# Optimization experiments

Hardware: AMD Instinct MI355X
Metric: run time of the kernel (lower is better)

Reference implementation:

```python
import jax, jax.numpy as jnp
import numpy as np

EPS = 1e-5
NHEAD = 8
NEG = -1e9  # matches -inf masked-fill semantics; rows never fully masked after fallback


def layer_norm(x, g, b):
    m = jnp.mean(x, axis=-1, keepdims=True)
    v = jnp.var(x, axis=-1, keepdims=True)
    return (x - m) * jax.lax.rsqrt(v + EPS) * g + b


def mha(q, k, v, Wqkv, bqkv, Wo, bo, bias=None):
    # torch nn.MultiheadAttention math (batch_first). Wqkv: [C, 3C] (jax layout).
    B, N, C = q.shape
    M = k.shape[1]
    d = C // NHEAD
    Wq, Wk, Wv = jnp.split(Wqkv, 3, axis=1)
    bq, bk, bv = jnp.split(bqkv, 3)
    qp = (q @ Wq + bq).reshape(B, N, NHEAD, d)
    kp = (k @ Wk + bk).reshape(B, M, NHEAD, d)
    vp = (v @ Wv + bv).reshape(B, M, NHEAD, d)
    s = jnp.einsum('bnhd,bmhd->bhnm', qp, kp) / np.sqrt(d).astype(q.dtype)
    if bias is not None:
        s = s + bias  # [B,1,N,M] broadcast over heads
    a = jax.nn.softmax(s, axis=-1)
    o = jnp.einsum('bhnm,bmhd->bnhd', a, vp).reshape(B, N, C)
    return o @ Wo + bo


def setup_inputs() -> dict:
    key = jax.random.key(0)
    B, Nq, HW, C, F = 8, 100, 4096, 512, 2048
    ks = jax.random.split(key, 16)
    s = 0.02
    inp = {
        'q': jax.random.normal(ks[0], (B, Nq, C), jnp.float32),
        'kv': jax.random.normal(ks[1], (B, HW, C), jnp.float32),
        'mask_bin': jax.random.randint(ks[2], (B, Nq, HW), 0, 2, jnp.int32),
        # MaskedXAttn: attn params + norm_q/norm_kv
        'xa_Wqkv': jax.random.normal(ks[3], (C, 3 * C), jnp.float32) * s,
        'xa_bqkv': jnp.zeros((3 * C,), jnp.float32),
        'xa_Wo': jax.random.normal(ks[4], (C, C), jnp.float32) * s,
        'xa_bo': jnp.zeros((C,), jnp.float32),
        'xa_gq': jnp.ones((C,), jnp.float32),
        'xa_bq_ln': jnp.zeros((C,), jnp.float32),
        'xa_gkv': jnp.ones((C,), jnp.float32),
        'xa_bkv_ln': jnp.zeros((C,), jnp.float32),
        # self-attention
        'sa_Wqkv': jax.random.normal(ks[5], (C, 3 * C), jnp.float32) * s,
        'sa_bqkv': jnp.zeros((3 * C,), jnp.float32),
        'sa_Wo': jax.random.normal(ks[6], (C, C), jnp.float32) * s,
        'sa_bo': jnp.zeros((C,), jnp.float32),
        # norms
        'n1_g': jnp.ones((C,), jnp.float32), 'n1_b': jnp.zeros((C,), jnp.float32),
        'n2_g': jnp.ones((C,), jnp.float32), 'n2_b': jnp.zeros((C,), jnp.float32),
        # FFN (MLP with num_layers=2: Linear(C,F), ReLU, Linear(F,C))
        'ff_W1': jax.random.normal(ks[7], (C, F), jnp.float32) * s,
        'ff_b1': jnp.zeros((F,), jnp.float32),
        'ff_W2': jax.random.normal(ks[8], (F, C), jnp.float32) * s,
        'ff_b2': jnp.zeros((C,), jnp.float32),
    }
    return inp


def reference(q, kv, mask_bin,
              xa_Wqkv, xa_bqkv, xa_Wo, xa_bo, xa_gq, xa_bq_ln, xa_gkv, xa_bkv_ln,
              sa_Wqkv, sa_bqkv, sa_Wo, sa_bo,
              n1_g, n1_b, n2_g, n2_b,
              ff_W1, ff_b1, ff_W2, ff_b2):
    # --- masked cross-attention (vectorized equivalent of per-query loop) ---
    qn = layer_norm(q, xa_gq, xa_bq_ln)
    kvn = layer_norm(kv, xa_gkv, xa_bkv_ln)
    allow = mask_bin.astype(bool)                      # [B,Nq,HW] True = attend
    row_any = jnp.any(allow, axis=-1, keepdims=True)   # queries with empty mask -> full attention
    eff = jnp.where(row_any, allow, True)
    bias = jnp.where(eff, 0.0, NEG).astype(q.dtype)[:, None, :, :]  # [B,1,Nq,HW]
    xa = mha(qn, kvn, kvn, xa_Wqkv, xa_bqkv, xa_Wo, xa_bo, bias=bias)
    q = q + xa
    # --- self-attention over queries ---
    qn1 = layer_norm(q, n1_g, n1_b)
    sa = mha(qn1, qn1, qn1, sa_Wqkv, sa_bqkv, sa_Wo, sa_bo)
    q = q + sa
    # --- FFN ---
    qn2 = layer_norm(q, n2_g, n2_b)
    h = jax.nn.relu(qn2 @ ff_W1 + ff_b1)
    q = q + (h @ ff_W2 + ff_b2)
    return q
```

## Files before the change

### kernel.cpp

```cpp
#include <hip/hip_runtime.h>

typedef unsigned short u16;
typedef unsigned int u32;
typedef __bf16 bf16x8 __attribute__((ext_vector_type(8)));
typedef short s16x4 __attribute__((ext_vector_type(4)));
typedef float f32x4 __attribute__((ext_vector_type(4)));

#define NEG_INF -3.0e38f
#define QSCALE 0.18033688011f

__device__ __forceinline__ u16 f2bf(float f){
  union { float f; u32 u; } v; v.f = f;
  u32 r = v.u + 0x7fffu + ((v.u >> 16) & 1u);
  return (u16)(r >> 16);
}
__device__ __forceinline__ float bf2f(u16 h){
  union { u32 u; float f; } v; v.u = ((u32)h) << 16; return v.f;
}
__device__ __forceinline__ short f2bf_s(float f){
  union { __bf16 h; short s; } cv; cv.h = (__bf16)f; return cv.s;
}

__device__ __forceinline__ f32x4 mfma16(s16x4 a, s16x4 b, f32x4 c){
#if __has_builtin(__builtin_amdgcn_mfma_f32_16x16x16bf16_1k)
  return __builtin_amdgcn_mfma_f32_16x16x16bf16_1k(a, b, c, 0, 0, 0);
#else
  asm("v_mfma_f32_16x16x16_bf16 %0, %1, %2, %0" : "+v"(c) : "v"(a), "v"(b));
  return c;
#endif
}

__device__ __forceinline__ void gl_lds16(const void* g, void* l){
  __builtin_amdgcn_global_load_lds((const __attribute__((address_space(1))) void*)g,
      (__attribute__((address_space(3))) void*)l, 16, 0, 0);
}

__device__ __forceinline__ void ln_body(const float* __restrict__ xr,
    const float* __restrict__ g, const float* __restrict__ b,
    u16* __restrict__ orow, int lane){
  float4 v0 = *(const float4*)(xr + lane * 4);
  float4 v1 = *(const float4*)(xr + 256 + lane * 4);
  float s = v0.x+v0.y+v0.z+v0.w + v1.x+v1.y+v1.z+v1.w;
  float q = v0.x*v0.x+v0.y*v0.y+v0.z*v0.z+v0.w*v0.w
          + v1.x*v1.x+v1.y*v1.y+v1.z*v1.z+v1.w*v1.w;
  #pragma unroll
  for (int d=1; d<64; d<<=1){ s += __shfl_xor(s, d, 64); q += __shfl_xor(q, d, 64); }
  float mean = s * (1.0f/512.0f);
  float var  = q * (1.0f/512.0f) - mean*mean;
  float rs = rsqrtf(var + 1e-5f);
  float4 g0 = *(const float4*)(g + lane*4), g1 = *(const float4*)(g + 256 + lane*4);
  float4 b0 = *(const float4*)(b + lane*4), b1 = *(const float4*)(b + 256 + lane*4);
  uint2 pa, pb;
  pa.x = (u32)f2bf((v0.x-mean)*rs*g0.x + b0.x) | ((u32)f2bf((v0.y-mean)*rs*g0.y + b0.y) << 16);
  pa.y = (u32)f2bf((v0.z-mean)*rs*g0.z + b0.z) | ((u32)f2bf((v0.w-mean)*rs*g0.w + b0.w) << 16);
  pb.x = (u32)f2bf((v1.x-mean)*rs*g1.x + b1.x) | ((u32)f2bf((v1.y-mean)*rs*g1.y + b1.y) << 16);
  pb.y = (u32)f2bf((v1.z-mean)*rs*g1.z + b1.z) | ((u32)f2bf((v1.w-mean)*rs*g1.w + b1.w) << 16);
  *(uint2*)(orow + lane*4) = pa;
  *(uint2*)(orow + 256 + lane*4) = pb;
}

__global__ __launch_bounds__(256) void ln_rows(const float* __restrict__ x,
    const float* __restrict__ g, const float* __restrict__ b,
    u16* __restrict__ out, int rows){
  int wid = threadIdx.x >> 6, lane = threadIdx.x & 63;
  int row = blockIdx.x * 4 + wid;
  if (row >= rows) return;
  ln_body(x + (size_t)row*512, g, b, out + (size_t)row*512, lane);
}

struct WtJobs {
  const float* W[7]; u16* Wt[7];
  int K[7], Nfull[7], ncol0[7], nt[7], blk0[7];
};
struct PrepArgs {
  WtJobs wt; int totW;
  const float *x0, *g0, *b0; u16* o0; int nb0, rows0;
  const float *x1, *g1, *b1; u16* o1; int nb1, rows1;
  const int* mask; u32* mw;
};

__global__ __launch_bounds__(256) void prep_all(PrepArgs P){
  __shared__ float tile[32][33];
  __shared__ unsigned long long blds[4];
  int bb = blockIdx.x;
  int tid = threadIdx.x;
  int wid = tid >> 6, lane = tid & 63;
  if (bb < P.totW){
    const WtJobs& J = P.wt;
    const float* W = J.W[0]; u16* Wt = J.Wt[0];
    int K = J.K[0], Nfull = J.Nfull[0], ncol0 = J.ncol0[0], nt = J.nt[0], blk0 = 0;
    #pragma unroll
    for (int i=1;i<7;i++)
      if (bb >= J.blk0[i]){
        W=J.W[i]; Wt=J.Wt[i]; K=J.K[i]; Nfull=J.Nfull[i]; ncol0=J.ncol0[i]; nt=J.nt[i]; blk0=J.blk0[i];
      }
    int lb = bb - blk0;
    int tk = lb / nt, tn = lb % nt;
    int col = tid & 31, kr = tid >> 5;
    #pragma unroll
    for (int i=0;i<4;i++){
      int k = tk*32 + kr + i*8;
      tile[kr + i*8][col] = W[(size_t)k*Nfull + ncol0 + tn*32 + col];
    }
    __syncthreads();
    int nl = tid >> 3, kc = (tid & 7) * 4;
    uint2 o;
    o.x = (u32)f2bf(tile[kc+0][nl]) | ((u32)f2bf(tile[kc+1][nl]) << 16);
    o.y = (u32)f2bf(tile[kc+2][nl]) | ((u32)f2bf(tile[kc+3][nl]) << 16);
    *(uint2*)(Wt + (size_t)(tn*32 + nl)*K + tk*32 + kc) = o;
  } else if (bb < P.totW + P.nb0){
    int row = (bb - P.totW)*4 + wid;
    if (row >= P.rows0) return;
    ln_body(P.x0 + (size_t)row*512, P.g0, P.b0, P.o0 + (size_t)row*512, lane);
  } else if (bb < P.totW + P.nb0 + P.nb1){
    int row = (bb - P.totW - P.nb0)*4 + wid;
    if (row >= P.rows1) return;
    ln_body(P.x1 + (size_t)row*512, P.g1, P.b1, P.o1 + (size_t)row*512, lane);
  } else {
    int lb = bb - P.totW - P.nb0 - P.nb1;
    int r0 = lb*2 + (wid >> 1);
    int word = tid & 127;
    const int* mr = P.mask + (size_t)r0*4096 + word*32;
    u32 w = 0;
    #pragma unroll
    for (int j=0;j<32;j+=4){
      int4 v = *(const int4*)(mr + j);
      w |= (u32)(v.x!=0) << j;
      w |= (u32)(v.y!=0) << (j+1);
      w |= (u32)(v.z!=0) << (j+2);
      w |= (u32)(v.w!=0) << (j+3);
    }
    blds[wid] = __ballot(w != 0);
    __syncthreads();
    bool any = (wid < 2) ? ((blds[0] | blds[1]) != 0ull) : ((blds[2] | blds[3]) != 0ull);
    P.mw[(size_t)r0*128 + word] = any ? w : 0xffffffffu;
  }
}

struct GemmJob {
  const u16* A; const u16* Bt; const float* bias;
  float* outf; u16* outb; const float* res; u16* out2;
  int M, N, K, lda, k0, ksplit, scale_cols, T1, rows_per_b, vstride, swz, brmap, blk0, nblk;
};
struct GemmJobs { GemmJob j[2]; int njobs; };

template<int EPI>
__device__ __forceinline__ void epi_store(const GemmJob& J, f32x4 (&acc)[4][4],
    int m0, int n0, int wm, int wn, int lg, int l15, int ksp){
  if (EPI == 3){
    float bv[4];
    #pragma unroll
    for (int ni=0;ni<4;ni++) bv[ni] = J.bias[n0 + wn*64 + ni*16 + l15];
    #pragma unroll
    for (int ni=0;ni<4;ni++){
      int c = n0 + wn*64 + ni*16 + l15;
      #pragma unroll
      for (int mi=0;mi<4;mi++){
        int mr0 = m0 + wm*64 + mi*16 + lg*4;
        if (mr0 >= J.M) continue;
        if (c < J.T1){
          #pragma unroll
          for (int r4=0;r4<4;r4++)
            J.outb[(size_t)(mr0+r4)*J.T1 + c] = f2bf(acc[mi][ni][r4] + bv[ni]);
        } else {
          int bidx = mr0 / J.rows_per_b;
          int key  = mr0 - bidx*J.rows_per_b;
          uint2 o;
          o.x = (u32)f2bf(acc[mi][ni][0]+bv[ni]) | ((u32)f2bf(acc[mi][ni][1]+bv[ni])<<16);
          o.y = (u32)f2bf(acc[mi][ni][2]+bv[ni]) | ((u32)f2bf(acc[mi][ni][3]+bv[ni])<<16);
          *(uint2*)(J.out2 + ((size_t)bidx*512 + (c - J.T1))*J.vstride + key) = o;
        }
      }
    }
  } else if (EPI == 4){
    #pragma unroll
    for (int mi=0;mi<4;mi++){
      #pragma unroll
      for (int r4=0;r4<4;r4++){
        int m = m0 + wm*64 + mi*16 + lg*4 + r4;
        if (m >= J.M) continue;
        float rb = J.bias[m];
        #pragma unroll
        for (int ni=0;ni<4;ni++){
          int c = n0 + wn*64 + ni*16 + l15;
          J.outb[(size_t)m*J.N + c] = f2bf(acc[mi][ni][r4] + rb);
        }
      }
    }
  } else if (EPI == 5){
    float* po_ = J.outf + (size_t)ksp*J.M*J.N;
    #pragma unroll
    for (int mi=0;mi<4;mi++){
      #pragma unroll
      for (int r4=0;r4<4;r4++){
        int m = m0 + wm*64 + mi*16 + lg*4 + r4;
        if (m >= J.M) continue;
        #pragma unroll
        for (int ni=0;ni<4;ni++){
          int c = n0 + wn*64 + ni*16 + l15;
          po_[(size_t)m*J.N + c] = acc[mi][ni][r4];
        }
      }
    }
  } else {
    float bv[4], scl[4];
    #pragma unroll
    for (int ni=0;ni<4;ni++){
      int c = n0 + wn*64 + ni*16 + l15;
      bv[ni]  = J.bias[c];
      scl[ni] = (c < J.scale_cols) ? QSCALE : 1.0f;
    }
    #pragma unroll
    for (int mi=0;mi<4;mi++){
      #pragma unroll
      for (int r4=0;r4<4;r4++){
        int m = m0 + wm*64 + mi*16 + lg*4 + r4;
        if (m >= J.M) continue;
        #pragma unroll
        for (int ni=0;ni<4;ni++){
          int c = n0 + wn*64 + ni*16 + l15;
          float v = acc[mi][ni][r4] + bv[ni];
          if (EPI == 0){
            J.outb[(size_t)m*J.N + c] = f2bf(v*scl[ni]);
          } else if (EPI == 1){
            J.outb[(size_t)m*J.N + c] = f2bf(fmaxf(v, 0.0f));
          } else {
            J.outf[(size_t)m*J.N + c] = v + J.res[(size_t)m*J.N + c];
          }
        }
      }
    }
  }
}

template<int EPIA, int EPIB>
__global__ __launch_bounds__(256) void gemm_multi(GemmJobs G){
  __shared__ __align__(16) u16 As[8192];
  __shared__ __align__(16) u16 Bs[8192];
  bool second = (G.njobs > 1) && ((int)blockIdx.x >= G.j[1].blk0);
  GemmJob J = second ? G.j[1] : G.j[0];
  int bid = (int)blockIdx.x - J.blk0;
  int ksp = 0;
  if (J.ksplit > 1){ ksp = bid / J.nblk; bid = bid % J.nblk; }
  if (J.swz){ int cpx = J.nblk >> 3; bid = (bid & 7)*cpx + (bid >> 3); }
  int NT = J.N >> 7;
  int mt = bid / NT, nt = bid % NT;
  int m0 = mt << 7, n0 = nt << 7;
  int kofs = J.k0 + ksp * J.K;
  int tid = threadIdx.x;
  int wid = tid >> 6, lane = tid & 63;
  int wm = wid >> 1, wn = wid & 1;
  int lg = lane >> 4, l15 = lane & 15;

  f32x4 acc[4][4] = {};
  int ktiles = J.K >> 6;
  for (int kt = 0; kt < ktiles; ++kt){
    int k0 = kofs + (kt << 6);
    if (kt) __syncthreads();
    #pragma unroll
    for (int i=0;i<4;i++){
      int L = i*4096 + tid*16;
      int T = L ^ (((L>>7)&7)<<4);
      int row = T >> 7, colb = T & 127;
      int ga = m0 + row; if (ga > J.M-1) ga = J.M-1;
      gl_lds16((const char*)J.A + ((size_t)ga*J.lda + k0)*2 + colb, (char*)As + L);
    }
    #pragma unroll
    for (int i=0;i<4;i++){
      int L = i*4096 + tid*16;
      int T = L ^ (((L>>7)&7)<<4);
      int row = T >> 7, colb = T & 127;
      int rowg = n0 + row;
      if (J.brmap){ int rb = rowg & 127; rowg = (rowg>>7)*J.brmap + (rb < J.brmap ? rb : J.brmap-1); }
      gl_lds16((const char*)J.Bt + ((size_t)rowg*J.lda + k0)*2 + colb, (char*)Bs + L);
    }
    __syncthreads();
    #pragma unroll
    for (int ks=0; ks<2; ++ks){
      bf16x8 af[4], bfr[4];
      #pragma unroll
      for (int mi=0; mi<4; ++mi){
        int r = wm*64 + mi*16 + l15;
        int byt = r*128 + ks*64 + lg*16;
        af[mi] = *(const bf16x8*)((const char*)As + (byt ^ ((r&7)<<4)));
      }
      #pragma unroll
      for (int ni=0; ni<4; ++ni){
        int r = wn*64 + ni*16 + l15;
        int byt = r*128 + ks*64 + lg*16;
        bfr[ni] = *(const bf16x8*)((const char*)Bs + (byt ^ ((r&7)<<4)));
      }
      __builtin_amdgcn_s_setprio(1);
      #pragma unroll
      for (int mi=0;mi<4;mi++)
        #pragma unroll
        for (int ni=0;ni<4;ni++)
          acc[mi][ni] = __builtin_amdgcn_mfma_f32_16x16x32_bf16(af[mi], bfr[ni], acc[mi][ni], 0,0,0);
      __builtin_amdgcn_s_setprio(0);
    }
  }

  if (second) epi_store<EPIB>(J, acc, m0, n0, wm, wn, lg, l15, ksp);
  else        epi_store<EPIA>(J, acc, m0, n0, wm, wn, lg, l15, ksp);
}

__global__ __launch_bounds__(256) void splitk_reduce(
    const float* __restrict__ part, int nsplit, const float* __restrict__ bias,
    const float* __restrict__ res, float* __restrict__ out, int N, int total4)
{
  int idx = (blockIdx.x*256 + threadIdx.x);
  if (idx >= total4) return;
  int e0 = idx*4;
  size_t MN = (size_t)total4*4;
  float4 a = *(const float4*)(part + e0);
  #pragma unroll
  for (int s=1;s<4;s++){
    float4 p = *(const float4*)(part + s*MN + e0);
    a.x += p.x; a.y += p.y; a.z += p.z; a.w += p.w;
  }
  float4 r = *(const float4*)(res + e0);
  int c = e0 & (N-1);
  float4 bv = *(const float4*)(bias + c);
  float4 o;
  o.x = a.x + r.x + bv.x; o.y = a.y + r.y + bv.y;
  o.z = a.z + r.z + bv.z; o.w = a.w + r.w + bv.w;
  *(float4*)(out + e0) = o;
}

template<bool PARTIAL, bool HASMASK, int NTILES>
__global__ __launch_bounds__(256) void attn_kernel(
    const u16* __restrict__ Qp, int ldq,
    const u16* __restrict__ Kp, int ldk, int kcol0,
    const u16* __restrict__ VT, size_t vbs, int vfs,
    const u32* __restrict__ maskw,
    float* __restrict__ pm, float* __restrict__ pl, u16* __restrict__ po,
    u16* __restrict__ o_out,
    int nq, int mk, int S, int H, int Bp, int swz)
{
  __shared__ __align__(16) u16 Ks[2*4096];
  __shared__ __align__(16) u16 Vs[2*4096];
  int bid = blockIdx.x;
  if (swz){ int cpx = gridDim.x >> 3; bid = (bid & 7)*cpx + (bid >> 3); }
  int s = bid % S; int h = (bid / S) % H; int b = bid / (S*H);
  int tid = threadIdx.x, wid = tid>>6, lane = tid&63;
  int lg = lane>>4, l15 = lane&15;
  int qbase = b*nq;
  int kps = mk / S;
  int kbeg = s * kps;
  int mwld = mk >> 5;
  int krel = lg*4;

  bf16x8 qf[2][2];
  #pragma unroll
  for (int mt=0;mt<2;mt++){
    int qr = wid*32 + mt*16 + l15; int qc = qr < nq ? qr : nq-1;
    #pragma unroll
    for (int ks=0;ks<2;ks++)
      qf[mt][ks] = *(const bf16x8*)(Qp + (size_t)(qbase+qc)*ldq + h*64 + ks*32 + lg*8);
  }
  u32 wmw[2][2*NTILES];
  if (HASMASK){
    #pragma unroll
    for (int mt=0;mt<2;mt++){
      int qc = (wid*32 + mt*16 + l15) < nq ? (wid*32 + mt*16 + l15) : nq-1;
      const u32* mrow = maskw + (size_t)(qbase+qc)*mwld + (kbeg>>5);
      #pragma unroll
      for (int wi=0; wi<2*NTILES; wi+=4){
        uint4 v = *(const uint4*)(mrow + wi);
        wmw[mt][wi+0]=v.x; wmw[mt][wi+1]=v.y; wmw[mt][wi+2]=v.z; wmw[mt][wi+3]=v.w;
      }
    }
  }

  float m_r[2] = {NEG_INF, NEG_INF};
  float l_r[2] = {0.0f, 0.0f};
  f32x4 of[2][4] = {};

  auto stage = [&](int t_, int bufi){
    int kb_ = kbeg + t_*64;
    #pragma unroll
    for (int i=0;i<2;i++){
      int idx = i*256 + tid;
      int key = idx>>3, sd = idx&7;
      int kc = kb_ + key; if (kc > mk-1) kc = mk-1;
      const char* src = (const char*)(Kp + (size_t)(b*mk + kc)*ldk + kcol0 + h*64) + ((sd ^ (key&7))<<4);
      gl_lds16(src, (char*)Ks + bufi*8192 + idx*16);
    }
    #pragma unroll
    for (int i=0;i<2;i++){
      int idx = i*256 + tid;
      int f = idx>>3, sd = idx&7;
      const char* src = (const char*)(VT + (size_t)b*vbs + (size_t)(h*64+f)*vfs + kb_) + ((sd ^ (f&7))<<4);
      gl_lds16(src, (char*)Vs + bufi*8192 + idx*16);
    }
  };

  stage(0, 0);

  #pragma unroll
  for (int t=0;t<NTILES;t++){
    if (t+1 < NTILES){
      stage(t+1, (t+1)&1);
      asm volatile("s_waitcnt vmcnt(4)" ::: "memory");
    } else {
      asm volatile("s_waitcnt vmcnt(0)" ::: "memory");
    }
    __builtin_amdgcn_s_barrier();

    const char* Kb = (const char*)Ks + (t&1)*8192;
    const char* Vb = (const char*)Vs + (t&1)*8192;
    int kb = kbeg + t*64;

    f32x4 sT[4][2] = {};
    #pragma unroll
    for (int nt2=0;nt2<4;nt2++){
      bf16x8 k0 = *(const bf16x8*)(Kb + ((nt2*16+l15)<<7) + (((lg  ) ^ (l15&7))<<4));
      bf16x8 k1 = *(const bf16x8*)(Kb + ((nt2*16+l15)<<7) + (((4+lg) ^ (l15&7))<<4));
      __builtin_amdgcn_s_setprio(1);
      #pragma unroll
      for (int mt=0;mt<2;mt++){
        sT[nt2][mt] = __builtin_amdgcn_mfma_f32_16x16x32_bf16(k0, qf[mt][0], sT[nt2][mt], 0,0,0);
        sT[nt2][mt] = __builtin_amdgcn_mfma_f32_16x16x32_bf16(k1, qf[mt][1], sT[nt2][mt], 0,0,0);
      }
      __builtin_amdgcn_s_setprio(0);
    }

    s16x4 pb[2][4];
    #pragma unroll
    for (int mt=0;mt<2;mt++){
      float mx = NEG_INF;
      #pragma unroll
      for (int nt2=0;nt2<4;nt2++){
        u32 wb = 0;
        if (HASMASK) wb = wmw[mt][t*2 + (nt2>>1)] >> (((nt2&1)<<4) + krel);
        #pragma unroll
        for (int r=0;r<4;r++){
          bool ok = HASMASK ? (((wb>>r)&1u) != 0) : (kb + nt2*16 + krel + r < mk);
          float sv = ok ? sT[nt2][mt][r] : NEG_INF;
          sT[nt2][mt][r] = sv;
          mx = fmaxf(mx, sv);
        }
      }
      mx = fmaxf(mx, __shfl_xor(mx, 16, 64));
      mx = fmaxf(mx, __shfl_xor(mx, 32, 64));
      if (!__all(mx <= m_r[mt] + 8.0f)){
        float mnew = fmaxf(m_r[mt], mx);
        float corr = exp2f(m_r[mt] - mnew);
        m_r[mt] = mnew;
        l_r[mt] *= corr;
        #pragma unroll
        for (int nf=0;nf<4;nf++) of[mt][nf] *= corr;
      }
      float ps = 0.0f;
      #pragma unroll
      for (int nt2=0;nt2<4;nt2++)
        #pragma unroll
        for (int r=0;r<4;r++){
          float p = exp2f(sT[nt2][mt][r] - m_r[mt]);
          ps += p;
          pb[mt][nt2][r] = f2bf_s(p);
        }
      ps += __shfl_xor(ps, 16, 64);
      ps += __shfl_xor(ps, 32, 64);
      l_r[mt] += ps;
    }

    #pragma unroll
    for (int nf=0;nf<4;nf++){
      s16x4 vf[4];
      #pragma unroll
      for (int nt2=0;nt2<4;nt2++){
        int slot = (nt2*2 + (lg>>1)) ^ (l15&7);
        vf[nt2] = *(const s16x4*)(Vb + ((nf*16+l15)<<7) + (slot<<4) + ((lg&1)<<3));
      }
      __builtin_amdgcn_s_setprio(1);
      #pragma unroll
      for (int mt=0;mt<2;mt++)
        #pragma unroll
        for (int nt2=0;nt2<4;nt2++)
          of[mt][nf] = mfma16(vf[nt2], pb[mt][nt2], of[mt][nf]);
      __builtin_amdgcn_s_setprio(0);
    }
    __builtin_amdgcn_s_barrier();
  }

  #pragma unroll
  for (int mt=0;mt<2;mt++){
    int q = wid*32 + mt*16 + l15;
    if (q < nq){
      if (PARTIAL){
        size_t base = (((size_t)(s*Bp + b)*H + h)*128 + q);
        if (lg == 0){ pm[base] = m_r[mt]; pl[base] = l_r[mt]; }
        #pragma unroll
        for (int nf=0;nf<4;nf++){
          uint2 o;
          o.x = (u32)f2bf(of[mt][nf][0]) | ((u32)f2bf(of[mt][nf][1])<<16);
          o.y = (u32)f2bf(of[mt][nf][2]) | ((u32)f2bf(of[mt][nf][3])<<16);
          *(uint2*)(po + base*64 + nf*16 + lg*4) = o;
        }
      } else {
        float inv = 1.0f / l_r[mt];
        #pragma unroll
        for (int nf=0;nf<4;nf++){
          uint2 o;
          o.x = (u32)f2bf(of[mt][nf][0]*inv) | ((u32)f2bf(of[mt][nf][1]*inv)<<16);
          o.y = (u32)f2bf(of[mt][nf][2]*inv) | ((u32)f2bf(of[mt][nf][3]*inv)<<16);
          *(uint2*)(o_out + (size_t)(qbase+q)*512 + h*64 + nf*16 + lg*4) = o;
        }
      }
    }
  }
}

__global__ __launch_bounds__(64) void attn_combine(
    const float* __restrict__ pm, const float* __restrict__ pl, const u16* __restrict__ po,
    u16* __restrict__ o_out, int S, int Bp, int H, int nq)
{
  int bid = blockIdx.x;
  int q = bid % nq; int h = (bid / nq) % H; int b = bid / (nq*H);
  int f = threadIdx.x;
  float mstar = NEG_INF;
  for (int s=0;s<S;s++){
    size_t idx = (((size_t)(s*Bp + b)*H + h)*128 + q);
    mstar = fmaxf(mstar, pm[idx]);
  }
  float L = 0.0f, acc = 0.0f;
  for (int s=0;s<S;s++){
    size_t idx = (((size_t)(s*Bp + b)*H + h)*128 + q);
    float w = exp2f(pm[idx] - mstar);
    L += w * pl[idx];
    acc += w * bf2f(po[idx*64 + f]);
  }
  o_out[((size_t)b*nq + q)*512 + h*64 + f] = f2bf(acc / L);
}

extern "C" void kernel_launch(void* const* d_in, const int* in_sizes, int n_in,
                              void* d_out, int out_size, void* d_ws, size_t ws_size,
                              hipStream_t stream){
  const float* q_in    = (const float*)d_in[0];
  const float* kv_in   = (const float*)d_in[1];
  const int*   maskb   = (const int*)d_in[2];
  const float* xa_Wqkv = (const float*)d_in[3];
  const float* xa_bqkv = (const float*)d_in[4];
  const float* xa_Wo   = (const float*)d_in[5];
  const float* xa_bo   = (const float*)d_in[6];
  const float* xa_gq   = (const float*)d_in[7];
  const float* xa_bq   = (const float*)d_in[8];
  const float* xa_gkv  = (const float*)d_in[9];
  const float* xa_bkv  = (const float*)d_in[10];
  const float* sa_Wqkv = (const float*)d_in[11];
  const float* sa_bqkv = (const float*)d_in[12];
  const float* sa_Wo   = (const float*)d_in[13];
  const float* sa_bo   = (const float*)d_in[14];
  const float* n1_g = (const float*)d_in[15];
  const float* n1_b = (const float*)d_in[16];
  const float* n2_g = (const float*)d_in[17];
  const float* n2_b = (const float*)d_in[18];
  const float* ff_W1 = (const float*)d_in[19];
  const float* ff_b1 = (const float*)d_in[20];
  const float* ff_W2 = (const float*)d_in[21];
  const float* ff_b2 = (const float*)d_in[22];

  char* ws = (char*)d_ws;
  size_t off = 0;
  auto alloc = [&](size_t bytes)->char*{ char* p = ws + off; off = (off + bytes + 255) & ~(size_t)255; return p; };
  u16* wq  = (u16*)alloc((size_t)512*512*2);
  u16* wkv = (u16*)alloc((size_t)1024*512*2);
  u16* wsa = (u16*)alloc((size_t)1536*512*2);
  u16* wxo = (u16*)alloc((size_t)512*512*2);
  u16* wso = (u16*)alloc((size_t)512*512*2);
  u16* wf1 = (u16*)alloc((size_t)2048*512*2);
  u16* wf2 = (u16*)alloc((size_t)512*2048*2);
  u16* qn  = (u16*)alloc((size_t)800*512*2);
  u16* qp  = (u16*)alloc((size_t)800*512*2);
  u32* mw  = (u32*)alloc((size_t)800*128*4);
  u16* kp  = (u16*)alloc((size_t)32768*512*2);
  u16* vpT = (u16*)alloc((size_t)8*512*4096*2);
  size_t reuse_off = off;
  u16* kvn = (u16*)alloc((size_t)32768*512*2);
  size_t offB = reuse_off;
  auto allocB = [&](size_t bytes)->char*{ char* p = ws + offB; offB = (offB + bytes + 255) & ~(size_t)255; return p; };
  const int S = 16;
  float* pm   = (float*)allocB((size_t)S*64*128*4);
  float* pl   = (float*)allocB((size_t)S*64*128*4);
  u16*   po   = (u16*)allocB((size_t)S*64*128*64*2);
  u16* o_xa   = (u16*)allocB((size_t)800*512*2);
  float* x1   = (float*)allocB((size_t)800*512*4);
  u16* qn1    = (u16*)allocB((size_t)800*512*2);
  u16* saqkv  = (u16*)allocB((size_t)800*1024*2);
  u16* vT2sa  = (u16*)allocB((size_t)512*1024*2);
  u16* o_sa   = (u16*)allocB((size_t)800*512*2);
  float* x2   = (float*)allocB((size_t)800*512*4);
  u16* qn2    = (u16*)allocB((size_t)800*512*2);
  u16* hbuf   = (u16*)allocB((size_t)800*2048*2);
  float* fpart = pm;

  PrepArgs P;
  P.wt.W[0]=xa_Wqkv; P.wt.Wt[0]=wq;  P.wt.K[0]=512;  P.wt.Nfull[0]=1536; P.wt.ncol0[0]=0;   P.wt.nt[0]=16;
  P.wt.W[1]=xa_Wqkv; P.wt.Wt[1]=wkv; P.wt.K[1]=512;  P.wt.Nfull[1]=1536; P.wt.ncol0[1]=512; P.wt.nt[1]=32;
  P.wt.W[2]=sa_Wqkv; P.wt.Wt[2]=wsa; P.wt.K[2]=512;  P.wt.Nfull[2]=1536; P.wt.ncol0[2]=0;   P.wt.nt[2]=48;
  P.wt.W[3]=xa_Wo;   P.wt.Wt[3]=wxo; P.wt.K[3]=512;  P.wt.Nfull[3]=512;  P.wt.ncol0[3]=0;   P.wt.nt[3]=16;
  P.wt.W[4]=sa_Wo;   P.wt.Wt[4]=wso; P.wt.K[4]=512;  P.wt.Nfull[4]=512;  P.wt.ncol0[4]=0;   P.wt.nt[4]=16;
  P.wt.W[5]=ff_W1;   P.wt.Wt[5]=wf1; P.wt.K[5]=512;  P.wt.Nfull[5]=2048; P.wt.ncol0[5]=0;   P.wt.nt[5]=64;
  P.wt.W[6]=ff_W2;   P.wt.Wt[6]=wf2; P.wt.K[6]=2048; P.wt.Nfull[6]=512;  P.wt.ncol0[6]=0;   P.wt.nt[6]=16;
  int tot = 0;
  for (int i=0;i<7;i++){ P.wt.blk0[i] = tot; tot += (P.wt.K[i]/32)*P.wt.nt[i]; }
  P.totW = tot;
  P.x0=q_in;  P.g0=xa_gq;  P.b0=xa_bq;  P.o0=qn;  P.nb0=200;  P.rows0=800;
  P.x1=kv_in; P.g1=xa_gkv; P.b1=xa_bkv; P.o1=kvn; P.nb1=8192; P.rows1=32768;
  P.mask=maskb; P.mw=mw;
  prep_all<<<tot + 200 + 8192 + 400, 256, 0, stream>>>(P);

  auto mkjob = [&](const u16*A, const u16*Bt, const float*bias, float*outf, u16*outb,
                   const float*res, u16*out2, int M, int N, int K, int lda, int k0,
                   int ksplit, int sc, int T1, int rpb, int vst, int swz, int brm,
                   int blk0, int nblk)->GemmJob{
    GemmJob j; j.A=A; j.Bt=Bt; j.bias=bias; j.outf=outf; j.outb=outb; j.res=res; j.out2=out2;
    j.M=M; j.N=N; j.K=K; j.lda=lda; j.k0=k0; j.ksplit=ksplit; j.scale_cols=sc; j.T1=T1;
    j.rows_per_b=rpb; j.vstride=vst; j.swz=swz; j.brmap=brm; j.blk0=blk0; j.nblk=nblk;
    return j;
  };

  {
    GemmJobs g;
    g.j[0] = mkjob(qn, wq, xa_bqkv, nullptr, qp, nullptr, nullptr,
                   800, 512, 512, 512, 0, 1, 512, 0,1,1, 0,0, 0, 28);
    g.j[1] = mkjob(kvn, wkv, xa_bqkv+512, nullptr, kp, nullptr, vpT,
                   32768, 1024, 512, 512, 0, 1, 0, 512, 4096, 4096, 1, 0, 28, 2048);
    g.njobs = 2;
    gemm_multi<0,3><<<28 + 2048, 256, 0, stream>>>(g);
  }
  attn_kernel<true,true,4><<<8*8*S, 256, 0, stream>>>(
      qp, 512, kp, 512, 0, vpT, (size_t)512*4096, 4096, mw,
      pm, pl, po, nullptr, 100, 4096, S, 8, 8, 1);
  attn_combine<<<8*8*100, 64, 0, stream>>>(pm, pl, po, o_xa, S, 8, 8, 100);
  {
    GemmJobs g;
    g.j[0] = mkjob(o_xa, wxo, xa_bo, x1, nullptr, q_in, nullptr,
                   800, 512, 512, 512, 0, 1, 0, 0,1,1, 0,0, 0, 28);
    g.j[1] = g.j[0]; g.njobs = 1;
    gemm_multi<2,2><<<28, 256, 0, stream>>>(g);
  }
  ln_rows<<<200, 256, 0, stream>>>(x1, n1_g, n1_b, qn1, 800);
  {
    GemmJobs g;
    g.j[0] = mkjob(qn1, wsa, sa_bqkv, nullptr, saqkv, nullptr, nullptr,
                   800, 1024, 512, 512, 0, 1, 512, 0,1,1, 0,0, 0, 56);
    g.j[1] = mkjob(wsa + (size_t)1024*512, qn1, sa_bqkv+1024, nullptr, vT2sa, nullptr, nullptr,
                   512, 1024, 512, 512, 0, 1, 0, 0,1,1, 0, 100, 56, 32);
    g.njobs = 2;
    gemm_multi<0,4><<<56 + 32, 256, 0, stream>>>(g);
  }
  attn_kernel<false,false,2><<<64, 256, 0, stream>>>(
      saqkv, 1024, saqkv, 1024, 512, vT2sa, (size_t)128, 1024, nullptr,
      nullptr, nullptr, nullptr, o_sa, 100, 100, 1, 8, 8, 0);
  {
    GemmJobs g;
    g.j[0] = mkjob(o_sa, wso, sa_bo, x2, nullptr, x1, nullptr,
                   800, 512, 512, 512, 0, 1, 0, 0,1,1, 0,0, 0, 28);
    g.j[1] = g.j[0]; g.njobs = 1;
    gemm_multi<2,2><<<28, 256, 0, stream>>>(g);
  }
  ln_rows<<<200, 256, 0, stream>>>(x2, n2_g, n2_b, qn2, 800);
  {
    GemmJobs g;
    g.j[0] = mkjob(qn2, wf1, ff_b1, nullptr, hbuf, nullptr, nullptr,
                   800, 2048, 512, 512, 0, 1, 0, 0,1,1, 0,0, 0, 112);
    g.j[1] = g.j[0]; g.njobs = 1;
    gemm_multi<1,1><<<112, 256, 0, stream>>>(g);
  }
  {
    GemmJobs g;
    g.j[0] = mkjob(hbuf, wf2, nullptr, fpart, nullptr, nullptr, nullptr,
                   800, 512, 512, 2048, 0, 4, 0, 0,1,1, 0,0, 0, 28);
    g.j[1] = g.j[0]; g.njobs = 1;
    gemm_multi<5,5><<<112, 256, 0, stream>>>(g);
  }
  splitk_reduce<<<(800*512/4 + 255)/256, 256, 0, stream>>>(
      fpart, 4, ff_b2, x2, (float*)d_out, 512, 800*512/4);
}
```

Before: 224.0 us.

## Fuse post-attention tail into one persistent kernel with grid barriers

Replaces the chain of small kernels after cross-attention (combine, output projection, layernorms, self-attention QKV, self-attention, FFN GEMMs, split-k reduce) with a single persistent kernel of 128 blocks. The stages are separated by atomic-counter grid barriers, and the barrier counters are reset by a memset before each launch. This removes roughly ten kernel launch gaps and tail-drain bubbles from a latency-bound stretch of small work. The costs are a spin-wait barrier per stage, some stages running with fewer blocks than before (the combine and reduce loops), and deadlock risk if the 128 blocks are not all resident at once.

After: 299.6 us. +33.8%, slower.

```diff
diff --git a/kernel.cpp b/kernel.cpp
--- a/kernel.cpp
+++ b/kernel.cpp
@@ -33,6 +33,17 @@
 __device__ __forceinline__ void gl_lds16(const void* g, void* l){
   __builtin_amdgcn_global_load_lds((const __attribute__((address_space(1))) void*)g,
       (__attribute__((address_space(3))) void*)l, 16, 0, 0);
+}
+
+__device__ __forceinline__ void gbar(u32* cnt, int ph, u32 nblk){
+  __syncthreads();
+  if (threadIdx.x == 0){
+    __threadfence();
+    atomicAdd(&cnt[ph], 1u);
+    while (atomicAdd(&cnt[ph], 0u) < nblk) __builtin_amdgcn_s_sleep(8);
+    __threadfence();
+  }
+  __syncthreads();
 }
 
 __device__ __forceinline__ void ln_body(const float* __restrict__ xr,
@@ -59,15 +70,6 @@
   *(uint2*)(orow + 256 + lane*4) = pb;
 }
 
-__global__ __launch_bounds__(256) void ln_rows(const float* __restrict__ x,
-    const float* __restrict__ g, const float* __restrict__ b,
-    u16* __restrict__ out, int rows){
-  int wid = threadIdx.x >> 6, lane = threadIdx.x & 63;
-  int row = blockIdx.x * 4 + wid;
-  if (row >= rows) return;
-  ln_body(x + (size_t)row*512, g, b, out + (size_t)row*512, lane);
-}
-
 struct WtJobs {
   const float* W[7]; u16* Wt[7];
   int K[7], Nfull[7], ncol0[7], nt[7], blk0[7];
@@ -233,13 +235,9 @@
   }
 }
 
-template<int EPIA, int EPIB>
-__global__ __launch_bounds__(256) void gemm_multi(GemmJobs G){
-  __shared__ __align__(16) u16 As[8192];
-  __shared__ __align__(16) u16 Bs[8192];
-  bool second = (G.njobs > 1) && ((int)blockIdx.x >= G.j[1].blk0);
-  GemmJob J = second ? G.j[1] : G.j[0];
-  int bid = (int)blockIdx.x - J.blk0;
+template<int EPI>
+__device__ __forceinline__ void gemm_block(const GemmJob& J, int bidIn, u16* As, u16* Bs){
+  int bid = bidIn;
   int ksp = 0;
   if (J.ksplit > 1){ ksp = bid / J.nblk; bid = bid % J.nblk; }
   if (J.swz){ int cpx = J.nblk >> 3; bid = (bid & 7)*cpx + (bid >> 3); }
@@ -299,48 +297,29 @@
       __builtin_amdgcn_s_setprio(0);
     }
   }
-
-  if (second) epi_store<EPIB>(J, acc, m0, n0, wm, wn, lg, l15, ksp);
-  else        epi_store<EPIA>(J, acc, m0, n0, wm, wn, lg, l15, ksp);
-}
-
-__global__ __launch_bounds__(256) void splitk_reduce(
-    const float* __restrict__ part, int nsplit, const float* __restrict__ bias,
-    const float* __restrict__ res, float* __restrict__ out, int N, int total4)
-{
-  int idx = (blockIdx.x*256 + threadIdx.x);
-  if (idx >= total4) return;
-  int e0 = idx*4;
-  size_t MN = (size_t)total4*4;
-  float4 a = *(const float4*)(part + e0);
-  #pragma unroll
-  for (int s=1;s<4;s++){
-    float4 p = *(const float4*)(part + s*MN + e0);
-    a.x += p.x; a.y += p.y; a.z += p.z; a.w += p.w;
-  }
-  float4 r = *(const float4*)(res + e0);
-  int c = e0 & (N-1);
-  float4 bv = *(const float4*)(bias + c);
-  float4 o;
-  o.x = a.x + r.x + bv.x; o.y = a.y + r.y + bv.y;
-  o.z = a.z + r.z + bv.z; o.w = a.w + r.w + bv.w;
-  *(float4*)(out + e0) = o;
+  epi_store<EPI>(J, acc, m0, n0, wm, wn, lg, l15, ksp);
+}
+
+template<int EPIA, int EPIB>
+__global__ __launch_bounds__(256) void gemm_multi(GemmJobs G){
+  __shared__ __align__(16) u16 As[8192];
+  __shared__ __align__(16) u16 Bs[8192];
+  bool second = (G.njobs > 1) && ((int)blockIdx.x >= G.j[1].blk0);
+  if (second) gemm_block<EPIB>(G.j[1], (int)blockIdx.x - G.j[1].blk0, As, Bs);
+  else        gemm_block<EPIA>(G.j[0], (int)blockIdx.x, As, Bs);
 }
 
 template<bool PARTIAL, bool HASMASK, int NTILES>
-__global__ __launch_bounds__(256) void attn_kernel(
+__device__ __forceinline__ void attn_block(
     const u16* __restrict__ Qp, int ldq,
     const u16* __restrict__ Kp, int ldk, int kcol0,
     const u16* __restrict__ VT, size_t vbs, int vfs,
     const u32* __restrict__ maskw,
     float* __restrict__ pm, float* __restrict__ pl, u16* __restrict__ po,
     u16* __restrict__ o_out,
-    int nq, int mk, int S, int H, int Bp, int swz)
+    int nq, int mk, int S, int H, int Bp, int swz, int bid, u16* Ks, u16* Vs)
 {
-  __shared__ __align__(16) u16 Ks[2*4096];
-  __shared__ __align__(16) u16 Vs[2*4096];
-  int bid = blockIdx.x;
-  if (swz){ int cpx = gridDim.x >> 3; bid = (bid & 7)*cpx + (bid >> 3); }
+  if (swz){ int cpx = S*H*Bp >> 3; bid = (bid & 7)*cpx + (bid >> 3); }
   int s = bid % S; int h = (bid / S) % H; int b = bid / (S*H);
   int tid = threadIdx.x, wid = tid>>6, lane = tid&63;
   int lg = lane>>4, l15 = lane&15;
@@ -512,26 +491,105 @@
   }
 }
 
-__global__ __launch_bounds__(64) void attn_combine(
-    const float* __restrict__ pm, const float* __restrict__ pl, const u16* __restrict__ po,
-    u16* __restrict__ o_out, int S, int Bp, int H, int nq)
+template<bool PARTIAL, bool HASMASK, int NTILES>
+__global__ __launch_bounds__(256) void attn_kernel(
+    const u16* Qp, int ldq, const u16* Kp, int ldk, int kcol0,
+    const u16* VT, size_t vbs, int vfs, const u32* maskw,
+    float* pm, float* pl, u16* po, u16* o_out,
+    int nq, int mk, int S, int H, int Bp, int swz)
 {
+  __shared__ __align__(16) u16 Ks[2*4096];
+  __shared__ __align__(16) u16 Vs[2*4096];
+  attn_block<PARTIAL,HASMASK,NTILES>(Qp,ldq,Kp,ldk,kcol0,VT,vbs,vfs,maskw,
+      pm,pl,po,o_out,nq,mk,S,H,Bp,swz,(int)blockIdx.x,Ks,Vs);
+}
+
+struct TailArgs {
+  const float* pm; const float* pl; const u16* po; u16* o_xa;
+  GemmJob jxo, jsaq, jsav, jso, jf1, jf2;
+  const float* x1; const float* n1g; const float* n1b; u16* qn1;
+  const float* x2; const float* n2g; const float* n2b; u16* qn2;
+  const u16* saqkv; u16* vT2sa; u16* o_sa;
+  const float* fpart; const float* ffb2; float* outp;
+  u32* bar;
+};
+
+__global__ __launch_bounds__(256) void tail_all(TailArgs A){
+  __shared__ __align__(16) u16 smem[16384];
+  u16* As = smem; u16* Bs = smem + 8192;
+  const u32 NB = 128;
   int bid = blockIdx.x;
-  int q = bid % nq; int h = (bid / nq) % H; int b = bid / (nq*H);
-  int f = threadIdx.x;
-  float mstar = NEG_INF;
-  for (int s=0;s<S;s++){
-    size_t idx = (((size_t)(s*Bp + b)*H + h)*128 + q);
-    mstar = fmaxf(mstar, pm[idx]);
-  }
-  float L = 0.0f, acc = 0.0f;
-  for (int s=0;s<S;s++){
-    size_t idx = (((size_t)(s*Bp + b)*H + h)*128 + q);
-    float w = exp2f(pm[idx] - mstar);
-    L += w * pl[idx];
-    acc += w * bf2f(po[idx*64 + f]);
-  }
-  o_out[((size_t)b*nq + q)*512 + h*64 + f] = f2bf(acc / L);
+  int tid = threadIdx.x;
+  int wid = tid >> 6, lane = tid & 63;
+
+  for (int g = bid*4 + wid; g < 6400; g += 512){
+    int q = g % 100, h = (g/100) & 7, b = g / 800;
+    float mstar = NEG_INF;
+    for (int s=0;s<16;s++){
+      size_t idx = (((size_t)(s*8 + b)*8 + h)*128 + q);
+      mstar = fmaxf(mstar, A.pm[idx]);
+    }
+    float L = 0.0f, acc = 0.0f;
+    for (int s=0;s<16;s++){
+      size_t idx = (((size_t)(s*8 + b)*8 + h)*128 + q);
+      float w = exp2f(A.pm[idx] - mstar);
+      L += w * A.pl[idx];
+      acc += w * bf2f(A.po[idx*64 + lane]);
+    }
+    A.o_xa[((size_t)b*100 + q)*512 + h*64 + lane] = f2bf(acc / L);
+  }
+  gbar(A.bar, 0, NB);
+
+  if (bid < 28) gemm_block<2>(A.jxo, bid, As, Bs);
+  gbar(A.bar, 1, NB);
+
+  for (int g = bid; g < 200; g += 128){
+    int row = g*4 + wid;
+    if (row < 800) ln_body(A.x1 + (size_t)row*512, A.n1g, A.n1b, A.qn1 + (size_t)row*512, lane);
+  }
+  gbar(A.bar, 2, NB);
+
+  if (bid < 56) gemm_block<0>(A.jsaq, bid, As, Bs);
+  else if (bid < 88) gemm_block<4>(A.jsav, bid - 56, As, Bs);
+  gbar(A.bar, 3, NB);
+
+  if (bid < 64)
+    attn_block<false,false,2>(A.saqkv, 1024, A.saqkv, 1024, 512,
+        A.vT2sa, (size_t)128, 1024, nullptr, nullptr, nullptr, nullptr,
+        A.o_sa, 100, 100, 1, 8, 8, 0, bid, As, Bs);
+  gbar(A.bar, 4, NB);
+
+  if (bid < 28) gemm_block<2>(A.jso, bid, As, Bs);
+  gbar(A.bar, 5, NB);
+
+  for (int g = bid; g < 200; g += 128){
+    int row = g*4 + wid;
+    if (row < 800) ln_body(A.x2 + (size_t)row*512, A.n2g, A.n2b, A.qn2 + (size_t)row*512, lane);
+  }
+  gbar(A.bar, 6, NB);
+
+  if (bid < 112) gemm_block<1>(A.jf1, bid, As, Bs);
+  gbar(A.bar, 7, NB);
+
+  if (bid < 112) gemm_block<5>(A.jf2, bid, As, Bs);
+  gbar(A.bar, 8, NB);
+
+  for (int i = bid*256 + tid; i < 102400; i += 128*256){
+    int e0 = i*4;
+    float4 a = *(const float4*)(A.fpart + e0);
+    #pragma unroll
+    for (int s=1;s<4;s++){
+      float4 p = *(const float4*)(A.fpart + (size_t)s*409600 + e0);
+      a.x += p.x; a.y += p.y; a.z += p.z; a.w += p.w;
+    }
+    float4 r = *(const float4*)(A.x2 + e0);
+    int c = e0 & 511;
+    float4 bv = *(const float4*)(A.ffb2 + c);
+    float4 o;
+    o.x = a.x + r.x + bv.x; o.y = a.y + r.y + bv.y;
+    o.z = a.z + r.z + bv.z; o.w = a.w + r.w + bv.w;
+    *(float4*)(A.outp + e0) = o;
+  }
 }
 
 extern "C" void kernel_launch(void* const* d_in, const int* in_sizes, int n_in,
@@ -574,6 +632,7 @@
   u16* qn  = (u16*)alloc((size_t)800*512*2);
   u16* qp  = (u16*)alloc((size_t)800*512*2);
   u32* mw  = (u32*)alloc((size_t)800*128*4);
+  u32* bar = (u32*)alloc(256);
   u16* kp  = (u16*)alloc((size_t)32768*512*2);
   u16* vpT = (u16*)alloc((size_t)8*512*4096*2);
   size_t reuse_off = off;
@@ -633,49 +692,26 @@
   attn_kernel<true,true,4><<<8*8*S, 256, 0, stream>>>(
       qp, 512, kp, 512, 0, vpT, (size_t)512*4096, 4096, mw,
       pm, pl, po, nullptr, 100, 4096, S, 8, 8, 1);
-  attn_combine<<<8*8*100, 64, 0, stream>>>(pm, pl, po, o_xa, S, 8, 8, 100);
-  {
-    GemmJobs g;
-    g.j[0] = mkjob(o_xa, wxo, xa_bo, x1, nullptr, q_in, nullptr,
-                   800, 512, 512, 512, 0, 1, 0, 0,1,1, 0,0, 0, 28);
-    g.j[1] = g.j[0]; g.njobs = 1;
-    gemm_multi<2,2><<<28, 256, 0, stream>>>(g);
-  }
-  ln_rows<<<200, 256, 0, stream>>>(x1, n1_g, n1_b, qn1, 800);
-  {
-    GemmJobs g;
-    g.j[0] = mkjob(qn1, wsa, sa_bqkv, nullptr, saqkv, nullptr, nullptr,
-                   800, 1024, 512, 512, 0, 1, 512, 0,1,1, 0,0, 0, 56);
-    g.j[1] = mkjob(wsa + (size_t)1024*512, qn1, sa_bqkv+1024, nullptr, vT2sa, nullptr, nullptr,
-                   512, 1024, 512, 512, 0, 1, 0, 0,1,1, 0, 100, 56, 32);
-    g.njobs = 2;
-    gemm_multi<0,4><<<56 + 32, 256, 0, stream>>>(g);
-  }
-  attn_kernel<false,false,2><<<64, 256, 0, stream>>>(
-      saqkv, 1024, saqkv, 1024, 512, vT2sa, (size_t)128, 1024, nullptr,
-      nullptr, nullptr, nullptr, o_sa, 100, 100, 1, 8, 8, 0);
-  {
-    GemmJobs g;
-    g.j[0] = mkjob(o_sa, wso, sa_bo, x2, nullptr, x1, nullptr,
-                   800, 512, 512, 512, 0, 1, 0, 0,1,1, 0,0, 0, 28);
-    g.j[1] = g.j[0]; g.njobs = 1;
-    gemm_multi<2,2><<<28, 256, 0, stream>>>(g);
-  }
-  ln_rows<<<200, 256, 0, stream>>>(x2, n2_g, n2_b, qn2, 800);
-  {
-    GemmJobs g;
-    g.j[0] = mkjob(qn2, wf1, ff_b1, nullptr, hbuf, nullptr, nullptr,
-                   800, 2048, 512, 512, 0, 1, 0, 0,1,1, 0,0, 0, 112);
-    g.j[1] = g.j[0]; g.njobs = 1;
-    gemm_multi<1,1><<<112, 256, 0, stream>>>(g);
-  }
-  {
-    GemmJobs g;
-    g.j[0] = mkjob(hbuf, wf2, nullptr, fpart, nullptr, nullptr, nullptr,
-                   800, 512, 512, 2048, 0, 4, 0, 0,1,1, 0,0, 0, 28);
-    g.j[1] = g.j[0]; g.njobs = 1;
-    gemm_multi<5,5><<<112, 256, 0, stream>>>(g);
-  }
-  splitk_reduce<<<(800*512/4 + 255)/256, 256, 0, stream>>>(
-      fpart, 4, ff_b2, x2, (float*)d_out, 512, 800*512/4);
-}
+
+  hipMemsetAsync(bar, 0, 64, stream);
+  TailArgs T;
+  T.pm = pm; T.pl = pl; T.po = po; T.o_xa = o_xa;
+  T.jxo  = mkjob(o_xa, wxo, xa_bo, x1, nullptr, q_in, nullptr,
+                 800, 512, 512, 512, 0, 1, 0, 0,1,1, 0,0, 0, 28);
+  T.jsaq = mkjob(qn1, wsa, sa_bqkv, nullptr, saqkv, nullptr, nullptr,
+                 800, 1024, 512, 512, 0, 1, 512, 0,1,1, 0,0, 0, 56);
+  T.jsav = mkjob(wsa + (size_t)1024*512, qn1, sa_bqkv+1024, nullptr, vT2sa, nullptr, nullptr,
+                 512, 1024, 512, 512, 0, 1, 0, 0,1,1, 0, 100, 0, 32);
+  T.jso  = mkjob(o_sa, wso, sa_bo, x2, nullptr, x1, nullptr,
+                 800, 512, 512, 512, 0, 1, 0, 0,1,1, 0,0, 0, 28);
+  T.jf1  = mkjob(qn2, wf1, ff_b1, nullptr, hbuf, nullptr, nullptr,
+                 800, 2048, 512, 512, 0, 1, 0, 0,1,1, 0,0, 0, 112);
+  T.jf2  = mkjob(hbuf, wf2, nullptr, fpart, nullptr, nullptr, nullptr,
+                 800, 512, 512, 2048, 0, 4, 0, 0,1,1, 0,0, 0, 28);
+  T.x1 = x1; T.n1g = n1_g; T.n1b = n1_b; T.qn1 = qn1;
+  T.x2 = x2; T.n2g = n2_g; T.n2b = n2_b; T.qn2 = qn2;
+  T.saqkv = saqkv; T.vT2sa = vT2sa; T.o_sa = o_sa;
+  T.fpart = fpart; T.ffb2 = ff_b2; T.outp = (float*)d_out;
+  T.bar = bar;
+  tail_all<<<128, 256, 0, stream>>>(T);
+}
```
